# Kernel tuning notes

Hardware: AMD Instinct MI355X
Metric: run time of the kernel (lower is better)

The kernel has to match this reference:

```python
import jax, jax.numpy as jnp
import numpy as np

B = 16384
LATENT = 64
COND = 6
H = 256
OUT = 3
NUM_LAYERS = 2
IN0 = OUT + LATENT + COND  # 73, LSTM layer-0 input size


def setup_inputs() -> dict:
    key = jax.random.key(0)
    ks = jax.random.split(key, 16)
    s = 0.05
    return {
        "z": jax.random.normal(ks[0], (B, LATENT), jnp.float32),
        "conditions": jax.random.normal(ks[1], (B, COND), jnp.float32),
        "fc_init_w": jax.random.normal(ks[2], (H * NUM_LAYERS, LATENT + COND), jnp.float32) * s,
        "fc_init_b": jax.random.normal(ks[3], (H * NUM_LAYERS,), jnp.float32) * s,
        "w_ih0": jax.random.normal(ks[4], (4 * H, IN0), jnp.float32) * s,
        "w_hh0": jax.random.normal(ks[5], (4 * H, H), jnp.float32) * s,
        "b_ih0": jax.random.normal(ks[6], (4 * H,), jnp.float32) * s,
        "b_hh0": jax.random.normal(ks[7], (4 * H,), jnp.float32) * s,
        "w_ih1": jax.random.normal(ks[8], (4 * H, H), jnp.float32) * s,
        "w_hh1": jax.random.normal(ks[9], (4 * H, H), jnp.float32) * s,
        "b_ih1": jax.random.normal(ks[10], (4 * H,), jnp.float32) * s,
        "b_hh1": jax.random.normal(ks[11], (4 * H,), jnp.float32) * s,
        "out_w1": jax.random.normal(ks[12], (H // 2, H), jnp.float32) * s,
        "out_b1": jax.random.normal(ks[13], (H // 2,), jnp.float32) * s,
        "out_w2": jax.random.normal(ks[14], (OUT, H // 2), jnp.float32) * s,
        "out_b2": jax.random.normal(ks[15], (OUT,), jnp.float32) * s,
        "seq_len": 50,
    }


def _lstm_cell(x, h, c, w_ih, w_hh, b_ih, b_hh):
    # PyTorch gate order: i, f, g, o
    gates = x @ w_ih.T + b_ih + h @ w_hh.T + b_hh  # [B, 4H]
    i, f, g, o = jnp.split(gates, 4, axis=-1)
    c_new = jax.nn.sigmoid(f) * c + jax.nn.sigmoid(i) * jnp.tanh(g)
    h_new = jax.nn.sigmoid(o) * jnp.tanh(c_new)
    return h_new, c_new


def reference(z, conditions, fc_init_w, fc_init_b,
              w_ih0, w_hh0, b_ih0, b_hh0,
              w_ih1, w_hh1, b_ih1, b_hh1,
              out_w1, out_b1, out_w2, out_b2, seq_len):
    batch = z.shape[0]
    zc = jnp.concatenate([z, conditions], axis=1)  # [B, latent+cond]
    init_h = (zc @ fc_init_w.T + fc_init_b).reshape(batch, NUM_LAYERS, H)
    h0, h1 = init_h[:, 0, :], init_h[:, 1, :]
    c0 = jnp.zeros_like(h0)
    c1 = jnp.zeros_like(h1)
    cur = conditions[:, :3]  # start waypoint as first input

    def step(carry, _):
        h0, c0, h1, c1, cur = carry
        x = jnp.concatenate([cur, z, conditions], axis=1)  # [B, IN0]
        h0n, c0n = _lstm_cell(x, h0, c0, w_ih0, w_hh0, b_ih0, b_hh0)
        h1n, c1n = _lstm_cell(h0n, h1, c1, w_ih1, w_hh1, b_ih1, b_hh1)
        hid = jax.nn.relu(h1n @ out_w1.T + out_b1)
        out = hid @ out_w2.T + out_b2  # [B, 3]
        return (h0n, c0n, h1n, c1n, out), out

    _, ys = jax.lax.scan(step, (h0, c0, h1, c1, cur), None, length=seq_len)
    return jnp.transpose(ys, (1, 0, 2))  # [B, seq_len, 3]
```

## Files before the change

kernel.cpp:

```cpp
#include <hip/hip_runtime.h>
#include <hip/hip_bf16.h>

typedef short short8 __attribute__((ext_vector_type(8)));
typedef float f32x4 __attribute__((ext_vector_type(4)));

#define BROWS 64
#define NTHR  512
#define XK    96
#define XSTR  104
#define HSTR  264
#define HIDSTR 129
#define NKT0  11
#define NKT1  16
#define NKTO  8
#define PK0_ELEMS (64*NKT0*512)
#define PK1_ELEMS (64*NKT1*512)
#define PKO_ELEMS (8*NKTO*512)

#define L_X    0
#define L_H    13312
#define HBUF   (BROWS*HSTR)
#define HBUF_B (HBUF*2)
#define L_HID  (L_H + 3*HBUF_B)
#define L_OW2  (L_HID + 33024)
#define L_OB2  (L_OW2 + 1536)
#define LDS_TOTAL 149264

__device__ inline unsigned short f2bf(float x){
  unsigned u = __float_as_uint(x);
  u += 0x7FFFu + ((u >> 16) & 1u);
  return (unsigned short)(u >> 16);
}
__device__ inline float bf2f(unsigned short s){ return __uint_as_float(((unsigned)s) << 16); }
__device__ inline float sigm(float x){ return 1.f / (1.f + __expf(-x)); }
__device__ inline float ftanh(float x){ float e = __expf(2.f*x); return 1.f - 2.f/(e + 1.f); }

__global__ void pack_weights(const float* __restrict__ wih0, const float* __restrict__ whh0,
                             const float* __restrict__ bih0, const float* __restrict__ bhh0,
                             const float* __restrict__ wih1, const float* __restrict__ whh1,
                             const float* __restrict__ ow1,
                             unsigned short* __restrict__ wsb){
  int idx = blockIdx.x * blockDim.x + threadIdx.x;
  int total = PK0_ELEMS + PK1_ELEMS + PKO_ELEMS;
  if (idx >= total) return;
  float w;
  size_t off;
  if (idx < PK0_ELEMS) {
    int nt = idx / (NKT0*512), rem = idx % (NKT0*512), kt = rem / 512, li = rem % 512;
    int lane = li >> 3, j = li & 7;
    int n = lane & 15, k = ((lane >> 4) << 3) + j;
    int Kg = kt*32 + k, g = nt*16 + n;
    if (Kg < 73)        w = wih0[g*73 + Kg];
    else if (Kg == 73)  w = bih0[g] + bhh0[g];
    else if (Kg < XK)   w = 0.f;
    else                w = whh0[g*256 + (Kg - XK)];
    off = ((size_t)(nt*NKT0 + kt)*64 + lane)*8 + j;
  } else if (idx < PK0_ELEMS + PK1_ELEMS) {
    int i2 = idx - PK0_ELEMS;
    int nt = i2 / (NKT1*512), rem = i2 % (NKT1*512), kt = rem / 512, li = rem % 512;
    int lane = li >> 3, j = li & 7;
    int n = lane & 15, k = ((lane >> 4) << 3) + j;
    int Kg = kt*32 + k, g = nt*16 + n;
    w = (Kg < 256) ? wih1[g*256 + Kg] : whh1[g*256 + (Kg - 256)];
    off = (size_t)PK0_ELEMS + ((size_t)(nt*NKT1 + kt)*64 + lane)*8 + j;
  } else {
    int i2 = idx - PK0_ELEMS - PK1_ELEMS;
    int nt = i2 / (NKTO*512), rem = i2 % (NKTO*512), kt = rem / 512, li = rem % 512;
    int lane = li >> 3, j = li & 7;
    int n = lane & 15, k = ((lane >> 4) << 3) + j;
    int Kg = kt*32 + k, uh = nt*16 + n;
    w = ow1[uh*256 + Kg];
    off = (size_t)PK0_ELEMS + (size_t)PK1_ELEMS + ((size_t)(nt*NKTO + kt)*64 + lane)*8 + j;
  }
  wsb[off] = f2bf(w);
}

__global__ void __launch_bounds__(NTHR, 1)
traj_main(const float* __restrict__ z, const float* __restrict__ cond,
          const float* __restrict__ fiw, const float* __restrict__ fib,
          const float* __restrict__ bih1, const float* __restrict__ bhh1,
          const float* __restrict__ ob1,  const float* __restrict__ ow2,
          const float* __restrict__ ob2,
          const unsigned short* __restrict__ wsb, const int* __restrict__ seqp,
          float* __restrict__ out){
  extern __shared__ char smem[];
  unsigned short* Xl  = (unsigned short*)(smem + L_X);
  unsigned short* Hl  = (unsigned short*)(smem + L_H);
  float*          HIDl= (float*)(smem + L_HID);
  float*          OW2l= (float*)(smem + L_OW2);
  float*          OB2l= (float*)(smem + L_OB2);

  const int tid = threadIdx.x, wv = tid >> 6, lane = tid & 63;
  const int bid = blockIdx.x;
  const int row0 = bid * BROWS;
  const int T = *seqp;

  const unsigned short* pk0i = wsb;
  const unsigned short* pk1i = wsb + (size_t)PK0_ELEMS;
  const unsigned short* pkoi = wsb + (size_t)PK0_ELEMS + (size_t)PK1_ELEMS;

  {
    int r = tid >> 3, seg = tid & 7;
    int gr = row0 + r;
    for (int c = seg*13; c < seg*13 + 13; ++c) {
      float v;
      if (c < 3)        v = cond[gr*6 + c];
      else if (c < 67)  v = z[gr*64 + (c - 3)];
      else if (c < 73)  v = cond[gr*6 + (c - 67)];
      else if (c == 73) v = 1.0f;
      else              v = 0.f;
      Xl[r*XSTR + c] = f2bf(v);
    }
  }
  if (tid < 384) OW2l[tid] = ow2[tid];
  if (tid < 3)   OB2l[tid] = ob2[tid];

  {
    int r = tid >> 3, ub = (tid & 7) * 32;
    int gr = row0 + r;
    #pragma unroll 1
    for (int u = ub; u < ub + 32; ++u) {
      float s0 = fib[u], s1 = fib[256 + u];
      const float* w0r = fiw + (size_t)u * 70;
      const float* w1r = fiw + (size_t)(256 + u) * 70;
      for (int jj = 0; jj < 64; ++jj) { float xv = z[gr*64 + jj]; s0 += xv * w0r[jj]; s1 += xv * w1r[jj]; }
      for (int jj = 0; jj < 6;  ++jj) { float xv = cond[gr*6 + jj]; s0 += xv * w0r[64 + jj]; s1 += xv * w1r[64 + jj]; }
      Hl[0*HBUF + r*HSTR + u] = f2bf(s0);
      Hl[1*HBUF + r*HSTR + u] = f2bf(s1);
    }
  }

  float bias1r[8];
  #pragma unroll
  for (int p = 0; p < 2; ++p) {
    int u = wv*32 + p*16 + (lane & 15);
    #pragma unroll
    for (int g = 0; g < 4; ++g)
      bias1r[p*4 + g] = bih1[g*256 + u] + bhh1[g*256 + u];
  }
  float ob1r = ob1[wv*16 + (lane & 15)];

  float c0s[32], c1s[32];
  #pragma unroll
  for (int i = 0; i < 32; ++i) { c0s[i] = 0.f; c1s[i] = 0.f; }

  __syncthreads();

  const int arow = lane & 15, koff = (lane >> 4) * 8;

  int ia = 0, ib = 1, ic = 2;

  for (int t = 0; t < T; ++t) {
    const unsigned short* Ha = Hl + ia*HBUF;
    const unsigned short* Hb = Hl + ib*HBUF;
    unsigned short*       Hc = Hl + ic*HBUF;
    unsigned short*       HaW= Hl + ia*HBUF;

    #pragma unroll
    for (int p = 0; p < 2; ++p) {
      const unsigned short* wb = pk0i + ((size_t)((wv*2 + p)*NKT0)*64 + lane)*8;

      short8 wh[3][4];
      #pragma unroll
      for (int g = 0; g < 4; ++g) {
        const unsigned short* q0 = wb + (size_t)g*(16*NKT0*512);
        wh[0][g] = *(const short8*)(q0);
        wh[1][g] = *(const short8*)(q0 + 512);
      }

      f32x4 acc[4][4];
      #pragma unroll
      for (int mt = 0; mt < 4; ++mt)
        #pragma unroll
        for (int g = 0; g < 4; ++g) acc[mt][g] = (f32x4){0.f, 0.f, 0.f, 0.f};

      #pragma unroll
      for (int kt = 0; kt < NKT0; ++kt) {
        const int cb = kt % 3, nb2 = (kt + 2) % 3;
        if (kt + 2 < NKT0) {
          #pragma unroll
          for (int g = 0; g < 4; ++g)
            wh[nb2][g] = *(const short8*)(wb + (size_t)g*(16*NKT0*512) + (size_t)(kt+2)*512);
        }
        short8 a[4];
        if (kt < 3) {
          #pragma unroll
          for (int mt = 0; mt < 4; ++mt)
            a[mt] = *(const short8*)(Xl + (mt*16 + arow)*XSTR + kt*32 + koff);
        } else {
          #pragma unroll
          for (int mt = 0; mt < 4; ++mt)
            a[mt] = *(const short8*)(Ha + (mt*16 + arow)*HSTR + (kt - 3)*32 + koff);
        }
        #pragma unroll
        for (int g = 0; g < 4; ++g)
          #pragma unroll
          for (int mt = 0; mt < 4; ++mt)
            acc[mt][g] = __builtin_amdgcn_mfma_f32_16x16x32_bf16(a[mt], wh[cb][g], acc[mt][g], 0, 0, 0);
      }

      const int u = wv*32 + p*16 + (lane & 15);
      #pragma unroll
      for (int mt = 0; mt < 4; ++mt) {
        #pragma unroll
        for (int q = 0; q < 4; ++q) {
          float iv = sigm(acc[mt][0][q]);
          float fv = sigm(acc[mt][1][q]);
          float gv = ftanh(acc[mt][2][q]);
          float ov = sigm(acc[mt][3][q]);
          float cn = fv * c0s[(p*4 + mt)*4 + q] + iv * gv;
          c0s[(p*4 + mt)*4 + q] = cn;
          float hn = ov * ftanh(cn);
          int r = mt*16 + ((lane >> 4) << 2) + q;
          Hc[r*HSTR + u] = f2bf(hn);
        }
      }
    }
    __syncthreads();

    #pragma unroll
    for (int p = 0; p < 2; ++p) {
      const unsigned short* wb = pk1i + ((size_t)((wv*2 + p)*NKT1)*64 + lane)*8;

      short8 wh[3][4];
      #pragma unroll
      for (int g = 0; g < 4; ++g) {
        const unsigned short* q0 = wb + (size_t)g*(16*NKT1*512);
        wh[0][g] = *(const short8*)(q0);
        wh[1][g] = *(const short8*)(q0 + 512);
      }

      f32x4 acc[4][4];
      #pragma unroll
      for (int mt = 0; mt < 4; ++mt)
        #pragma unroll
        for (int g = 0; g < 4; ++g) {
          float b = bias1r[p*4 + g];
          acc[mt][g] = (f32x4){b, b, b, b};
        }

      #pragma unroll
      for (int kt = 0; kt < NKT1; ++kt) {
        const int cb = kt % 3, nb2 = (kt + 2) % 3;
        if (kt + 2 < NKT1) {
          #pragma unroll
          for (int g = 0; g < 4; ++g)
            wh[nb2][g] = *(const short8*)(wb + (size_t)g*(16*NKT1*512) + (size_t)(kt+2)*512);
        }
        short8 a[4];
        if (kt < 8) {
          #pragma unroll
          for (int mt = 0; mt < 4; ++mt)
            a[mt] = *(const short8*)(Hc + (mt*16 + arow)*HSTR + kt*32 + koff);
        } else {
          #pragma unroll
          for (int mt = 0; mt < 4; ++mt)
            a[mt] = *(const short8*)(Hb + (mt*16 + arow)*HSTR + (kt - 8)*32 + koff);
        }
        #pragma unroll
        for (int g = 0; g < 4; ++g)
          #pragma unroll
          for (int mt = 0; mt < 4; ++mt)
            acc[mt][g] = __builtin_amdgcn_mfma_f32_16x16x32_bf16(a[mt], wh[cb][g], acc[mt][g], 0, 0, 0);
      }

      const int u = wv*32 + p*16 + (lane & 15);
      #pragma unroll
      for (int mt = 0; mt < 4; ++mt) {
        #pragma unroll
        for (int q = 0; q < 4; ++q) {
          float iv = sigm(acc[mt][0][q]);
          float fv = sigm(acc[mt][1][q]);
          float gv = ftanh(acc[mt][2][q]);
          float ov = sigm(acc[mt][3][q]);
          float cn = fv * c1s[(p*4 + mt)*4 + q] + iv * gv;
          c1s[(p*4 + mt)*4 + q] = cn;
          float hn = ov * ftanh(cn);
          int r = mt*16 + ((lane >> 4) << 2) + q;
          HaW[r*HSTR + u] = f2bf(hn);
        }
      }
    }
    __syncthreads();

    {
      const unsigned short* wb = pkoi + ((size_t)(wv*NKTO)*64 + lane)*8;
      short8 wh[3];
      wh[0] = *(const short8*)(wb);
      wh[1] = *(const short8*)(wb + 512);

      f32x4 acc3[4];
      #pragma unroll
      for (int mt = 0; mt < 4; ++mt) acc3[mt] = (f32x4){ob1r, ob1r, ob1r, ob1r};

      #pragma unroll
      for (int kt = 0; kt < NKTO; ++kt) {
        const int cb = kt % 3, nb2 = (kt + 2) % 3;
        if (kt + 2 < NKTO)
          wh[nb2] = *(const short8*)(wb + (size_t)(kt+2)*512);
        short8 a[4];
        #pragma unroll
        for (int mt = 0; mt < 4; ++mt)
          a[mt] = *(const short8*)(HaW + (mt*16 + arow)*HSTR + kt*32 + koff);
        #pragma unroll
        for (int mt = 0; mt < 4; ++mt)
          acc3[mt] = __builtin_amdgcn_mfma_f32_16x16x32_bf16(a[mt], wh[cb], acc3[mt], 0, 0, 0);
      }
      const int uh = wv*16 + (lane & 15);
      #pragma unroll
      for (int mt = 0; mt < 4; ++mt)
        #pragma unroll
        for (int q = 0; q < 4; ++q) {
          float hv = fmaxf(acc3[mt][q], 0.f);
          int r = mt*16 + ((lane >> 4) << 2) + q;
          HIDl[r*HIDSTR + uh] = hv;
        }
    }
    __syncthreads();

    {
      int r = tid >> 3, e = tid & 7;
      const float* hrow = HIDl + r*HIDSTR + e*16;
      float s0 = 0.f, s1 = 0.f, s2 = 0.f;
      #pragma unroll
      for (int k = 0; k < 16; ++k) {
        float hv = hrow[k];
        int kk = e*16 + k;
        s0 += hv * OW2l[kk];
        s1 += hv * OW2l[128 + kk];
        s2 += hv * OW2l[256 + kk];
      }
      #pragma unroll
      for (int d = 4; d; d >>= 1) {
        s0 += __shfl_down(s0, d, 8);
        s1 += __shfl_down(s1, d, 8);
        s2 += __shfl_down(s2, d, 8);
      }
      if (e == 0) {
        s0 += OB2l[0]; s1 += OB2l[1]; s2 += OB2l[2];
        int gr = row0 + r;
        float* orow = out + (size_t)gr * (T*3) + t*3;
        orow[0] = s0; orow[1] = s1; orow[2] = s2;
        Xl[r*XSTR + 0] = f2bf(s0);
        Xl[r*XSTR + 1] = f2bf(s1);
        Xl[r*XSTR + 2] = f2bf(s2);
      }
    }
    __syncthreads();

    int tmp = ia; ia = ic; ic = ib; ib = tmp;
  }
}

extern "C" void kernel_launch(void* const* d_in, const int* in_sizes, int n_in,
                              void* d_out, int out_size, void* d_ws, size_t ws_size,
                              hipStream_t stream){
  const float* z    = (const float*)d_in[0];
  const float* cond = (const float*)d_in[1];
  const float* fiw  = (const float*)d_in[2];
  const float* fib  = (const float*)d_in[3];
  const float* wih0 = (const float*)d_in[4];
  const float* whh0 = (const float*)d_in[5];
  const float* bih0 = (const float*)d_in[6];
  const float* bhh0 = (const float*)d_in[7];
  const float* wih1 = (const float*)d_in[8];
  const float* whh1 = (const float*)d_in[9];
  const float* bih1 = (const float*)d_in[10];
  const float* bhh1 = (const float*)d_in[11];
  const float* ow1  = (const float*)d_in[12];
  const float* ob1  = (const float*)d_in[13];
  const float* ow2  = (const float*)d_in[14];
  const float* ob2  = (const float*)d_in[15];
  const int*   seqp = (const int*)d_in[16];
  unsigned short* wsb = (unsigned short*)d_ws;
  float* outp = (float*)d_out;

  hipFuncSetAttribute((const void*)traj_main,
                      hipFuncAttributeMaxDynamicSharedMemorySize, LDS_TOTAL);

  int packtot = PK0_ELEMS + PK1_ELEMS + PKO_ELEMS;
  pack_weights<<<(packtot + 255)/256, 256, 0, stream>>>(wih0, whh0, bih0, bhh0,
                                                        wih1, whh1, ow1, wsb);
  traj_main<<<16384/BROWS, NTHR, LDS_TOTAL, stream>>>(z, cond, fiw, fib,
                                                      bih1, bhh1,
                                                      ob1, ow2, ob2, wsb, seqp, outp);
}
```

Measured before the change: 5.732 ms.

## Halve rows per block to run two workgroups per CU

Cuts the batch rows handled per workgroup from 64 to 32, which halves LDS use and the register-held accumulators and cell state. Launch bounds now request two blocks per CU, so twice as many blocks are launched and latency can be hidden across them. Weight prefetch depth also drops from two k-tiles ahead to one. The cost is that each weight tile loaded from global or L2 now feeds only two M-tiles instead of four, roughly doubling total weight traffic, and the shallower prefetch may expose more load latency.

```diff
diff --git a/kernel.cpp b/kernel.cpp
--- a/kernel.cpp
+++ b/kernel.cpp
@@ -4,7 +4,7 @@
 typedef short short8 __attribute__((ext_vector_type(8)));
 typedef float f32x4 __attribute__((ext_vector_type(4)));
 
-#define BROWS 64
+#define BROWS 32
 #define NTHR  512
 #define XK    96
 #define XSTR  104
@@ -18,13 +18,13 @@
 #define PKO_ELEMS (8*NKTO*512)
 
 #define L_X    0
-#define L_H    13312
+#define L_H    6656
 #define HBUF   (BROWS*HSTR)
 #define HBUF_B (HBUF*2)
 #define L_HID  (L_H + 3*HBUF_B)
-#define L_OW2  (L_HID + 33024)
+#define L_OW2  (L_HID + BROWS*HIDSTR*4)
 #define L_OB2  (L_OW2 + 1536)
-#define LDS_TOTAL 149264
+#define LDS_TOTAL 75408
 
 __device__ inline unsigned short f2bf(float x){
   unsigned u = __float_as_uint(x);
@@ -75,7 +75,7 @@
   wsb[off] = f2bf(w);
 }
 
-__global__ void __launch_bounds__(NTHR, 1)
+__global__ void __launch_bounds__(NTHR, 2)
 traj_main(const float* __restrict__ z, const float* __restrict__ cond,
           const float* __restrict__ fiw, const float* __restrict__ fib,
           const float* __restrict__ bih1, const float* __restrict__ bhh1,
@@ -100,9 +100,9 @@
   const unsigned short* pkoi = wsb + (size_t)PK0_ELEMS + (size_t)PK1_ELEMS;
 
   {
-    int r = tid >> 3, seg = tid & 7;
+    int r = tid >> 4, seg = tid & 15;
     int gr = row0 + r;
-    for (int c = seg*13; c < seg*13 + 13; ++c) {
+    for (int c = seg*7; c < seg*7 + 7 && c < XSTR; ++c) {
       float v;
       if (c < 3)        v = cond[gr*6 + c];
       else if (c < 67)  v = z[gr*64 + (c - 3)];
@@ -116,10 +116,10 @@
   if (tid < 3)   OB2l[tid] = ob2[tid];
 
   {
-    int r = tid >> 3, ub = (tid & 7) * 32;
+    int r = tid >> 4, ub = (tid & 15) * 16;
     int gr = row0 + r;
     #pragma unroll 1
-    for (int u = ub; u < ub + 32; ++u) {
+    for (int u = ub; u < ub + 16; ++u) {
       float s0 = fib[u], s1 = fib[256 + u];
       const float* w0r = fiw + (size_t)u * 70;
       const float* w1r = fiw + (size_t)(256 + u) * 70;
@@ -133,16 +133,16 @@
   float bias1r[8];
   #pragma unroll
   for (int p = 0; p < 2; ++p) {
-    int u = wv*32 + p*16 + (lane & 15);
+    int u = (wv*2 + p)*16 + (lane & 15);
     #pragma unroll
     for (int g = 0; g < 4; ++g)
       bias1r[p*4 + g] = bih1[g*256 + u] + bhh1[g*256 + u];
   }
   float ob1r = ob1[wv*16 + (lane & 15)];
 
-  float c0s[32], c1s[32];
+  float c0s[16], c1s[16];
   #pragma unroll
-  for (int i = 0; i < 32; ++i) { c0s[i] = 0.f; c1s[i] = 0.f; }
+  for (int i = 0; i < 16; ++i) { c0s[i] = 0.f; c1s[i] = 0.f; }
 
   __syncthreads();
 
@@ -160,56 +160,53 @@
     for (int p = 0; p < 2; ++p) {
       const unsigned short* wb = pk0i + ((size_t)((wv*2 + p)*NKT0)*64 + lane)*8;
 
-      short8 wh[3][4];
-      #pragma unroll
-      for (int g = 0; g < 4; ++g) {
-        const unsigned short* q0 = wb + (size_t)g*(16*NKT0*512);
-        wh[0][g] = *(const short8*)(q0);
-        wh[1][g] = *(const short8*)(q0 + 512);
-      }
-
-      f32x4 acc[4][4];
-      #pragma unroll
-      for (int mt = 0; mt < 4; ++mt)
+      short8 wh[2][4];
+      #pragma unroll
+      for (int g = 0; g < 4; ++g)
+        wh[0][g] = *(const short8*)(wb + (size_t)g*(16*NKT0*512));
+
+      f32x4 acc[2][4];
+      #pragma unroll
+      for (int mt = 0; mt < 2; ++mt)
         #pragma unroll
         for (int g = 0; g < 4; ++g) acc[mt][g] = (f32x4){0.f, 0.f, 0.f, 0.f};
 
       #pragma unroll
       for (int kt = 0; kt < NKT0; ++kt) {
-        const int cb = kt % 3, nb2 = (kt + 2) % 3;
-        if (kt + 2 < NKT0) {
+        const int cb = kt & 1, nb = cb ^ 1;
+        if (kt + 1 < NKT0) {
           #pragma unroll
           for (int g = 0; g < 4; ++g)
-            wh[nb2][g] = *(const short8*)(wb + (size_t)g*(16*NKT0*512) + (size_t)(kt+2)*512);
-        }
-        short8 a[4];
+            wh[nb][g] = *(const short8*)(wb + (size_t)g*(16*NKT0*512) + (size_t)(kt+1)*512);
+        }
+        short8 a[2];
         if (kt < 3) {
           #pragma unroll
-          for (int mt = 0; mt < 4; ++mt)
+          for (int mt = 0; mt < 2; ++mt)
             a[mt] = *(const short8*)(Xl + (mt*16 + arow)*XSTR + kt*32 + koff);
         } else {
           #pragma unroll
-          for (int mt = 0; mt < 4; ++mt)
+          for (int mt = 0; mt < 2; ++mt)
             a[mt] = *(const short8*)(Ha + (mt*16 + arow)*HSTR + (kt - 3)*32 + koff);
         }
         #pragma unroll
         for (int g = 0; g < 4; ++g)
           #pragma unroll
-          for (int mt = 0; mt < 4; ++mt)
+          for (int mt = 0; mt < 2; ++mt)
             acc[mt][g] = __builtin_amdgcn_mfma_f32_16x16x32_bf16(a[mt], wh[cb][g], acc[mt][g], 0, 0, 0);
       }
 
-      const int u = wv*32 + p*16 + (lane & 15);
-      #pragma unroll
-      for (int mt = 0; mt < 4; ++mt) {
+      const int u = (wv*2 + p)*16 + (lane & 15);
+      #pragma unroll
+      for (int mt = 0; mt < 2; ++mt) {
         #pragma unroll
         for (int q = 0; q < 4; ++q) {
           float iv = sigm(acc[mt][0][q]);
           float fv = sigm(acc[mt][1][q]);
           float gv = ftanh(acc[mt][2][q]);
           float ov = sigm(acc[mt][3][q]);
-          float cn = fv * c0s[(p*4 + mt)*4 + q] + iv * gv;
-          c0s[(p*4 + mt)*4 + q] = cn;
+          float cn = fv * c0s[(p*2 + mt)*4 + q] + iv * gv;
+          c0s[(p*2 + mt)*4 + q] = cn;
           float hn = ov * ftanh(cn);
           int r = mt*16 + ((lane >> 4) << 2) + q;
           Hc[r*HSTR + u] = f2bf(hn);
@@ -222,17 +219,14 @@
     for (int p = 0; p < 2; ++p) {
       const unsigned short* wb = pk1i + ((size_t)((wv*2 + p)*NKT1)*64 + lane)*8;
 
-      short8 wh[3][4];
-      #pragma unroll
-      for (int g = 0; g < 4; ++g) {
-        const unsigned short* q0 = wb + (size_t)g*(16*NKT1*512);
-        wh[0][g] = *(const short8*)(q0);
-        wh[1][g] = *(const short8*)(q0 + 512);
-      }
-
-      f32x4 acc[4][4];
-      #pragma unroll
-      for (int mt = 0; mt < 4; ++mt)
+      short8 wh[2][4];
+      #pragma unroll
+      for (int g = 0; g < 4; ++g)
+        wh[0][g] = *(const short8*)(wb + (size_t)g*(16*NKT1*512));
+
+      f32x4 acc[2][4];
+      #pragma unroll
+      for (int mt = 0; mt < 2; ++mt)
         #pragma unroll
         for (int g = 0; g < 4; ++g) {
           float b = bias1r[p*4 + g];
@@ -241,40 +235,40 @@
 
       #pragma unroll
       for (int kt = 0; kt < NKT1; ++kt) {
-        const int cb = kt % 3, nb2 = (kt + 2) % 3;
-        if (kt + 2 < NKT1) {
+        const int cb = kt & 1, nb = cb ^ 1;
+        if (kt + 1 < NKT1) {
           #pragma unroll
           for (int g = 0; g < 4; ++g)
-            wh[nb2][g] = *(const short8*)(wb + (size_t)g*(16*NKT1*512) + (size_t)(kt+2)*512);
-        }
-        short8 a[4];
+            wh[nb][g] = *(const short8*)(wb + (size_t)g*(16*NKT1*512) + (size_t)(kt+1)*512);
+        }
+        short8 a[2];
         if (kt < 8) {
           #pragma unroll
-          for (int mt = 0; mt < 4; ++mt)
+          for (int mt = 0; mt < 2; ++mt)
             a[mt] = *(const short8*)(Hc + (mt*16 + arow)*HSTR + kt*32 + koff);
         } else {
           #pragma unroll
-          for (int mt = 0; mt < 4; ++mt)
+          for (int mt = 0; mt < 2; ++mt)
             a[mt] = *(const short8*)(Hb + (mt*16 + arow)*HSTR + (kt - 8)*32 + koff);
         }
         #pragma unroll
         for (int g = 0; g < 4; ++g)
           #pragma unroll
-          for (int mt = 0; mt < 4; ++mt)
+          for (int mt = 0; mt < 2; ++mt)
             acc[mt][g] = __builtin_amdgcn_mfma_f32_16x16x32_bf16(a[mt], wh[cb][g], acc[mt][g], 0, 0, 0);
       }
 
-      const int u = wv*32 + p*16 + (lane & 15);
-      #pragma unroll
-      for (int mt = 0; mt < 4; ++mt) {
+      const int u = (wv*2 + p)*16 + (lane & 15);
+      #pragma unroll
+      for (int mt = 0; mt < 2; ++mt) {
         #pragma unroll
         for (int q = 0; q < 4; ++q) {
           float iv = sigm(acc[mt][0][q]);
           float fv = sigm(acc[mt][1][q]);
           float gv = ftanh(acc[mt][2][q]);
           float ov = sigm(acc[mt][3][q]);
-          float cn = fv * c1s[(p*4 + mt)*4 + q] + iv * gv;
-          c1s[(p*4 + mt)*4 + q] = cn;
+          float cn = fv * c1s[(p*2 + mt)*4 + q] + iv * gv;
+          c1s[(p*2 + mt)*4 + q] = cn;
           float hn = ov * ftanh(cn);
           int r = mt*16 + ((lane >> 4) << 2) + q;
           HaW[r*HSTR + u] = f2bf(hn);
@@ -285,30 +279,29 @@
 
     {
       const unsigned short* wb = pkoi + ((size_t)(wv*NKTO)*64 + lane)*8;
-      short8 wh[3];
+      short8 wh[2];
       wh[0] = *(const short8*)(wb);
-      wh[1] = *(const short8*)(wb + 512);
-
-      f32x4 acc3[4];
-      #pragma unroll
-      for (int mt = 0; mt < 4; ++mt) acc3[mt] = (f32x4){ob1r, ob1r, ob1r, ob1r};
+
+      f32x4 acc3[2];
+      #pragma unroll
+      for (int mt = 0; mt < 2; ++mt) acc3[mt] = (f32x4){ob1r, ob1r, ob1r, ob1r};
 
       #pragma unroll
       for (int kt = 0; kt < NKTO; ++kt) {
-        const int cb = kt % 3, nb2 = (kt + 2) % 3;
-        if (kt + 2 < NKTO)
-          wh[nb2] = *(const short8*)(wb + (size_t)(kt+2)*512);
-        short8 a[4];
-        #pragma unroll
-        for (int mt = 0; mt < 4; ++mt)
+        const int cb = kt & 1, nb = cb ^ 1;
+        if (kt + 1 < NKTO)
+          wh[nb] = *(const short8*)(wb + (size_t)(kt+1)*512);
+        short8 a[2];
+        #pragma unroll
+        for (int mt = 0; mt < 2; ++mt)
           a[mt] = *(const short8*)(HaW + (mt*16 + arow)*HSTR + kt*32 + koff);
         #pragma unroll
-        for (int mt = 0; mt < 4; ++mt)
+        for (int mt = 0; mt < 2; ++mt)
           acc3[mt] = __builtin_amdgcn_mfma_f32_16x16x32_bf16(a[mt], wh[cb], acc3[mt], 0, 0, 0);
       }
       const int uh = wv*16 + (lane & 15);
       #pragma unroll
-      for (int mt = 0; mt < 4; ++mt)
+      for (int mt = 0; mt < 2; ++mt)
         #pragma unroll
         for (int q = 0; q < 4; ++q) {
           float hv = fmaxf(acc3[mt][q], 0.f);
@@ -319,22 +312,22 @@
     __syncthreads();
 
     {
-      int r = tid >> 3, e = tid & 7;
-      const float* hrow = HIDl + r*HIDSTR + e*16;
+      int r = tid >> 4, e = tid & 15;
+      const float* hrow = HIDl + r*HIDSTR + e*8;
       float s0 = 0.f, s1 = 0.f, s2 = 0.f;
       #pragma unroll
-      for (int k = 0; k < 16; ++k) {
+      for (int k = 0; k < 8; ++k) {
         float hv = hrow[k];
-        int kk = e*16 + k;
+        int kk = e*8 + k;
         s0 += hv * OW2l[kk];
         s1 += hv * OW2l[128 + kk];
         s2 += hv * OW2l[256 + kk];
       }
       #pragma unroll
-      for (int d = 4; d; d >>= 1) {
-        s0 += __shfl_down(s0, d, 8);
-        s1 += __shfl_down(s1, d, 8);
-        s2 += __shfl_down(s2, d, 8);
+      for (int d = 8; d; d >>= 1) {
+        s0 += __shfl_down(s0, d, 16);
+        s1 += __shfl_down(s1, d, 16);
+        s2 += __shfl_down(s2, d, 16);
       }
       if (e == 0) {
         s0 += OB2l[0]; s1 += OB2l[1]; s2 += OB2l[2];
```

Result: slower. 9.902 ms (+72.8%).
